# Kernel tuning notes

Measured on AMD Instinct MI355X. Metric: run time of the kernel, lower is better.

Reference implementation:

```python
import jax, jax.numpy as jnp
import numpy as np

# Config: options = {hid_size:1280, num_lstm_layers:2, vocab_size:32000, dropout:0}
L, B, S, H, V = 2, 2, 512, 1280, 32000
C = H  # cell_size == hidden_size == input_size in BiLMEncoder(hid, hid, hid, L)


def setup_inputs() -> dict:
    key = jax.random.key(0)
    ks = jax.random.split(key, 11)
    sc = jnp.float32(0.05)
    def p(k, shape):
        return jax.random.normal(k, shape, dtype=jnp.float32) * sc
    return {
        "x": jax.random.normal(ks[0], (B, S, H), dtype=jnp.float32),
        "Wi_f": p(ks[1], (L, H, 4 * C)),   # input_linearity (no bias)
        "Ws_f": p(ks[2], (L, H, 4 * C)),   # state_linearity
        "b_f":  p(ks[3], (L, 4 * C)),      # state_linearity bias
        "Wp_f": p(ks[4], (L, C, H)),       # state_projection (no bias)
        "Wi_b": p(ks[5], (L, H, 4 * C)),
        "Ws_b": p(ks[6], (L, H, 4 * C)),
        "b_b":  p(ks[7], (L, 4 * C)),
        "Wp_b": p(ks[8], (L, C, H)),
        "W_lin": p(ks[9], (H, V)),
        "b_lin": p(ks[10], (V,)),
    }


def _lstm_dir(x, Wi, Ws, b, Wp, reverse):
    """LstmCellWithProjection over time. x: (B,S,H) -> (B,S,H)."""
    if reverse:
        x = x[:, ::-1, :]
    xp = jnp.einsum('bsh,hk->sbk', x, Wi)  # precompute input projections (S,B,4C)
    h0 = jnp.zeros((x.shape[0], H), x.dtype)
    c0 = jnp.zeros((x.shape[0], C), x.dtype)

    def step(carry, xt):
        h, c = carry
        g = xt + h @ Ws + b                      # (B,4C)
        i, f, z, o = jnp.split(g, 4, axis=-1)
        c_new = jax.nn.sigmoid(i) * jnp.tanh(z) + jax.nn.sigmoid(f) * c
        h_new = (jax.nn.sigmoid(o) * jnp.tanh(c_new)) @ Wp  # projected state
        return (h_new, c_new), h_new

    _, ys = jax.lax.scan(step, (h0, c0), xp)
    ys = jnp.transpose(ys, (1, 0, 2))  # (B,S,H)
    if reverse:
        ys = ys[:, ::-1, :]
    return ys


def _bilm(x, Wi_f, Ws_f, b_f, Wp_f, Wi_b, Ws_b, b_b, Wp_b):
    """ElmoLstm stacked bidirectional LSTM-with-projection, all-ones mask."""
    fwd_in, bwd_in = x, x
    outs = []
    for l in range(L):
        f_cache, b_cache = fwd_in, bwd_in
        f_out = _lstm_dir(fwd_in, Wi_f[l], Ws_f[l], b_f[l], Wp_f[l], reverse=False)
        b_out = _lstm_dir(bwd_in, Wi_b[l], Ws_b[l], b_b[l], Wp_b[l], reverse=True)
        if l != 0:  # residual skip between layers (ElmoLstm)
            f_out = f_out + f_cache
            b_out = b_out + b_cache
        fwd_in, bwd_in = f_out, b_out
        outs.append(jnp.concatenate([f_out, b_out], axis=-1))
    return jnp.stack(outs, axis=0)  # (L,B,S,2H)


def reference(x, Wi_f, Ws_f, b_f, Wp_f, Wi_b, Ws_b, b_b, Wp_b, W_lin, b_lin):
    enc = _bilm(x, Wi_f, Ws_f, b_f, Wp_f, Wi_b, Ws_b, b_b, Wp_b)
    fwd, bwd = enc[..., :H], enc[..., H:]
    logits_fwd = (jnp.einsum('lbsh,hv->lbsv', fwd, W_lin) + b_lin).reshape(B * S, -1)
    logits_bwd = (jnp.einsum('lbsh,hv->lbsv', bwd, W_lin) + b_lin).reshape(B * S, -1)
    return jnp.concatenate([logits_fwd, logits_bwd], axis=0)  # (2*B*S, L*V)
```

## Files before the change

kernel.cpp:

```cpp
#include <hip/hip_runtime.h>
#include <hip/hip_fp16.h>
#include <stdint.h>

#define S_LEN 512
#define HD 1280
#define GD 5120
#define VOC 32000

typedef __attribute__((ext_vector_type(8))) short short8;
typedef __attribute__((ext_vector_type(8))) _Float16 half8;
typedef __attribute__((ext_vector_type(4))) float floatx4;
typedef __attribute__((ext_vector_type(2))) _Float16 halfx2;
typedef __attribute__((ext_vector_type(4))) _Float16 halfx4;

#define GLB1 const __attribute__((address_space(1))) void*
#define LDS3 __attribute__((address_space(3))) void*

static __device__ __forceinline__ unsigned short f2h(float f) {
  return __builtin_bit_cast(unsigned short, (_Float16)f);
}
static __device__ __forceinline__ float h2f(unsigned short h) {
  return (float)__builtin_bit_cast(_Float16, h);
}
static __device__ __forceinline__ float tanhf_fast(float x) {
  float xc = fminf(fmaxf(x, -15.f), 15.f);
  float e = __expf(2.f * xc);
  return (e - 1.f) / (e + 1.f);
}
#if __has_builtin(__builtin_amdgcn_fdot2)
static __device__ __forceinline__ float fdot2(halfx2 a, halfx2 b, float c) {
  return __builtin_amdgcn_fdot2(a, b, c, false);
}
#else
static __device__ __forceinline__ float fdot2(halfx2 a, halfx2 b, float c) {
  return c + (float)a[0]*(float)b[0] + (float)a[1]*(float)b[1];
}
#endif

__global__ __launch_bounds__(256)
void transpose_cvt(const float* __restrict__ in, unsigned short* __restrict__ out,
                   int R, int C)
{
  __shared__ float tile[32][33];
  const int c0 = blockIdx.x * 32;
  const int r0 = blockIdx.y * 32;
  const int tx = threadIdx.x & 31;
  const int ty = threadIdx.x >> 5;
#pragma unroll
  for (int p = 0; p < 4; p++) {
    int rl = ty + p * 8;
    tile[rl][tx] = in[(size_t)(r0 + rl) * C + c0 + tx];
  }
  __syncthreads();
#pragma unroll
  for (int p = 0; p < 4; p++) {
    int cl = ty + p * 8;
    out[(size_t)(c0 + cl) * R + r0 + tx] = f2h(tile[tx][cl]);
  }
}

template<int AFP32, int CMODE>
__global__ __launch_bounds__(256, 2)
void gemm_k(const void* __restrict__ Ap, const unsigned short* __restrict__ BTp,
            void* __restrict__ Cp, const float* __restrict__ bias,
            const unsigned short* __restrict__ resid,
            int M, int N, int K, int rev)
{
  __shared__ __align__(16) short As[128 * 32];
  __shared__ __align__(16) short Bs[128 * 32];
  const int tid  = threadIdx.x;
  const int row0 = blockIdx.y * 128;
  const int col0 = blockIdx.x * 128;
  const int lane = tid & 63;
  const int wid  = tid >> 6;
  const int wrow = (wid >> 1) * 64;
  const int wcol = (wid & 1) * 64;
  const int lr   = lane & 15;
  const int gg   = lane >> 4;

  floatx4 acc[4][4];
#pragma unroll
  for (int m = 0; m < 4; m++)
#pragma unroll
    for (int n = 0; n < 4; n++)
      acc[m][n] = (floatx4)0.0f;

  for (int k0 = 0; k0 < K; k0 += 32) {
    __syncthreads();
#pragma unroll
    for (int p = 0; p < 2; p++) {
      int idx = p * 256 + tid;
      int r = idx >> 2, c = idx & 3;
      if constexpr (AFP32) {
        const float* src = (const float*)Ap + (size_t)(row0 + r) * K + k0 + c * 8;
        floatx4 f0 = *(const floatx4*)src;
        floatx4 f1 = *(const floatx4*)(src + 4);
        short8 va;
        va[0] = (short)f2h(f0[0]); va[1] = (short)f2h(f0[1]);
        va[2] = (short)f2h(f0[2]); va[3] = (short)f2h(f0[3]);
        va[4] = (short)f2h(f1[0]); va[5] = (short)f2h(f1[1]);
        va[6] = (short)f2h(f1[2]); va[7] = (short)f2h(f1[3]);
        *(short8*)&As[r * 32 + ((c ^ (r & 3)) * 8)] = va;
      } else {
        const unsigned short* gsa =
          (const unsigned short*)Ap + (size_t)(row0 + r) * K + k0 + ((c ^ (r & 3)) * 8);
        __builtin_amdgcn_global_load_lds((GLB1)gsa, (LDS3)&As[idx * 8], 16, 0, 0);
      }
      const unsigned short* gsb =
        BTp + (size_t)(col0 + r) * K + k0 + ((c ^ (r & 3)) * 8);
      __builtin_amdgcn_global_load_lds((GLB1)gsb, (LDS3)&Bs[idx * 8], 16, 0, 0);
    }
    __syncthreads();
    short8 af[4], bfv[4];
#pragma unroll
    for (int m = 0; m < 4; m++) {
      int r = wrow + m * 16 + lr;
      af[m] = *(const short8*)&As[r * 32 + ((gg ^ (r & 3)) * 8)];
    }
#pragma unroll
    for (int n = 0; n < 4; n++) {
      int c = wcol + n * 16 + lr;
      bfv[n] = *(const short8*)&Bs[c * 32 + ((gg ^ (c & 3)) * 8)];
    }
#pragma unroll
    for (int m = 0; m < 4; m++)
#pragma unroll
      for (int n = 0; n < 4; n++)
        acc[m][n] = __builtin_amdgcn_mfma_f32_16x16x32_f16(
            __builtin_bit_cast(half8, af[m]), __builtin_bit_cast(half8, bfv[n]),
            acc[m][n], 0, 0, 0);
  }

#pragma unroll
  for (int m = 0; m < 4; m++) {
    int rbase = row0 + wrow + m * 16 + 4 * gg;
#pragma unroll
    for (int n = 0; n < 4; n++) {
      int col = col0 + wcol + n * 16 + lr;
      if constexpr (CMODE == 1) {
        halfx4 t4;
#pragma unroll
        for (int i = 0; i < 4; i++) t4[i] = (_Float16)acc[m][n][i];
        *(halfx4*)((_Float16*)Cp + (size_t)col * M + rbase) = t4;
      } else if constexpr (CMODE == 0) {
        float bv = bias[col];
#pragma unroll
        for (int i = 0; i < 4; i++) {
          int r = rbase + i;
          int b = r >> 9, s = r & 511;
          int so = rev ? (511 - s) : s;
          ((float*)Cp)[(size_t)((so << 1) | b) * GD + col] = acc[m][n][i] + bv;
        }
      } else if constexpr (CMODE == 2) {
#pragma unroll
        for (int i = 0; i < 4; i++) {
          int r = rbase + i;
          int t = r >> 1, b = r & 1;
          int s = rev ? (511 - t) : t;
          size_t o = (size_t)((b << 9) | s) * HD + col;
          float v = acc[m][n][i];
          if (resid) v += h2f(resid[o]);
          ((unsigned short*)Cp)[o] = f2h(v);
        }
      } else {
        float bv = bias[col];
#pragma unroll
        for (int i = 0; i < 4; i++)
          ((float*)Cp)[(size_t)(rbase + i) * N + col] = acc[m][n][i] + bv;
      }
    }
  }
}

__global__ __launch_bounds__(256, 1)
void lstm_scan(const _Float16* __restrict__ wfT,
               const float* __restrict__ xp,
               unsigned short* __restrict__ Pout,
               unsigned int* __restrict__ pbuf,
               unsigned int* __restrict__ ctr,
               int tbase)
{
  const int dir = blockIdx.x & 1;
  const int g   = blockIdx.x >> 1;
  const int jbase = g * 10;
  const int tid = threadIdx.x;
  const int ks  = tid & 31;
  const int cg  = tid >> 5;

  __shared__ __align__(16) unsigned int wlds[40 * 640];
  __shared__ __align__(16) unsigned int plds[1280];
  __shared__ float gvals[40][2];

#pragma unroll 1
  for (int i = 0; i < 25; i++) {
    int idx = i * 256 + tid;
    int c = idx / 160, r = idx - c * 160;
    size_t rowIdx = (size_t)dir * GD + (c / 10) * HD + jbase + (c % 10);
    const uint4* src = (const uint4*)(wfT + rowIdx * HD);
    *(uint4*)&wlds[c * 640 + r * 4] = src[r];
  }

  int gcol[5];
#pragma unroll
  for (int i = 0; i < 5; i++) {
    int c = cg * 5 + i;
    gcol[i] = (c / 10) * HD + jbase + (c % 10);
  }
  const bool isRed = (ks == 0);

  const bool isOwn = tid < 10;
  const int ob = tid & 1;
  const int op = tid >> 1;
  float cst0 = 0.f, cst1 = 0.f;

  __syncthreads();

  for (int t = 0; t < S_LEN; t++) {
    float xpv[5][2];
    if (isRed) {
#pragma unroll
      for (int i = 0; i < 5; i++)
#pragma unroll
        for (int b = 0; b < 2; b++)
          xpv[i][b] = xp[((size_t)dir * 1024 + t * 2 + b) * GD + gcol[i]];
    }

    if (t > 0) {
      if (tid < 64) {
        const unsigned tgt = (unsigned)(tbase + t) * 4u;
        const unsigned int* cp = ctr + dir * 32 + (tid & 31);
        while (true) {
          unsigned v = __hip_atomic_load(cp, __ATOMIC_RELAXED, __HIP_MEMORY_SCOPE_AGENT);
          if (__all(v >= tgt)) break;
          __builtin_amdgcn_s_sleep(1);
        }
      }
      __syncthreads();
    }

    const unsigned int* pr = pbuf + (dir * 2 + (t & 1)) * 1280;
#pragma unroll
    for (int r = 0; r < 5; r++)
      plds[r * 256 + tid] = __hip_atomic_load(pr + r * 256 + tid,
                                              __ATOMIC_RELAXED, __HIP_MEMORY_SCOPE_AGENT);
    __syncthreads();

    float acc[5][2];
#pragma unroll
    for (int i = 0; i < 5; i++) { acc[i][0] = 0.f; acc[i][1] = 0.f; }
#pragma unroll
    for (int j = 0; j < 5; j++) {
      half8 pv0 = *(const half8*)&plds[0 * 640 + ks * 20 + j * 4];
      half8 pv1 = *(const half8*)&plds[1 * 640 + ks * 20 + j * 4];
#pragma unroll
      for (int i = 0; i < 5; i++) {
        half8 wv = *(const half8*)&wlds[(cg * 5 + i) * 640 + ks * 20 + j * 4];
#pragma unroll
        for (int u = 0; u < 4; u++) {
          halfx2 w2  = {wv[2 * u], wv[2 * u + 1]};
          halfx2 p02 = {pv0[2 * u], pv0[2 * u + 1]};
          halfx2 p12 = {pv1[2 * u], pv1[2 * u + 1]};
          acc[i][0] = fdot2(p02, w2, acc[i][0]);
          acc[i][1] = fdot2(p12, w2, acc[i][1]);
        }
      }
    }

#pragma unroll
    for (int i = 0; i < 5; i++)
#pragma unroll
      for (int b = 0; b < 2; b++) {
        float v = acc[i][b];
#pragma unroll
        for (int off = 16; off >= 1; off >>= 1)
          v += __shfl_xor(v, off, 32);
        if (isRed) gvals[cg * 5 + i][b] = v + xpv[i][b];
      }
    __syncthreads();

    unsigned packed = 0;
    if (isOwn) {
      int j0 = op * 2, j1 = op * 2 + 1;
      float gi0 = gvals[j0][ob],      gi1 = gvals[j1][ob];
      float gf0 = gvals[10 + j0][ob], gf1 = gvals[10 + j1][ob];
      float gz0 = gvals[20 + j0][ob], gz1 = gvals[20 + j1][ob];
      float go0 = gvals[30 + j0][ob], go1 = gvals[30 + j1][ob];
      float si0 = 1.f / (1.f + __expf(-gi0)), si1 = 1.f / (1.f + __expf(-gi1));
      float sf0 = 1.f / (1.f + __expf(-gf0)), sf1 = 1.f / (1.f + __expf(-gf1));
      float so0 = 1.f / (1.f + __expf(-go0)), so1 = 1.f / (1.f + __expf(-go1));
      cst0 = si0 * tanhf_fast(gz0) + sf0 * cst0;
      cst1 = si1 * tanhf_fast(gz1) + sf1 * cst1;
      float pv0 = so0 * tanhf_fast(cst0);
      float pv1 = so1 * tanhf_fast(cst1);
      packed = (unsigned)f2h(pv0) | ((unsigned)f2h(pv1) << 16);
      unsigned int* pw = pbuf + (dir * 2 + ((t + 1) & 1)) * 1280;
      __hip_atomic_store(pw + ob * 640 + (jbase >> 1) + op, packed,
                         __ATOMIC_RELAXED, __HIP_MEMORY_SCOPE_AGENT);
    }
    asm volatile("s_waitcnt vmcnt(0)" ::: "memory");
    if (tid == 0) {
      __hip_atomic_fetch_add(ctr + dir * 32 + (g & 31), 1u,
                             __ATOMIC_RELAXED, __HIP_MEMORY_SCOPE_AGENT);
    }
    if (isOwn)
      ((unsigned int*)Pout)[(((size_t)dir * 1024 + t * 2 + ob) * HD + jbase) / 2 + op] = packed;
  }
}

extern "C" void kernel_launch(void* const* d_in, const int* in_sizes, int n_in,
                              void* d_out, int out_size, void* d_ws, size_t ws_size,
                              hipStream_t stream)
{
  char* W = (char*)d_ws;
  const size_t WS_T  = 0;
  const size_t WI_T  = 52428800;
  const size_t WP_T  = 104857600;
  const size_t WF_T  = 117964800;
  const size_t HCAT  = 170393600;
  const size_t P_O   = 180879360;
  const size_t XP_O  = 186122240;
  const size_t PB_O  = 228065280;
  const size_t CTR_O = 228106240;
  const size_t NEED  = 228106496;
  const size_t WLIN_T = 0;
  if (ws_size < NEED) return;

  const float* x    = (const float*)d_in[0];
  const float* Wi_f = (const float*)d_in[1];
  const float* Ws_f = (const float*)d_in[2];
  const float* b_f  = (const float*)d_in[3];
  const float* Wp_f = (const float*)d_in[4];
  const float* Wi_b = (const float*)d_in[5];
  const float* Ws_b = (const float*)d_in[6];
  const float* b_b  = (const float*)d_in[7];
  const float* Wp_b = (const float*)d_in[8];
  const float* Wlin = (const float*)d_in[9];
  const float* blin = (const float*)d_in[10];

  hipMemsetAsync(W + PB_O, 0, 40960 + 256, stream);

  for (int l = 0; l < 2; l++)
    for (int d = 0; d < 2; d++) {
      int ld = l * 2 + d;
      const float* ws_src = (d ? Ws_b : Ws_f) + (size_t)l * HD * GD;
      const float* wi_src = (d ? Wi_b : Wi_f) + (size_t)l * HD * GD;
      const float* wp_src = (d ? Wp_b : Wp_f) + (size_t)l * HD * HD;
      transpose_cvt<<<dim3(GD / 32, HD / 32), 256, 0, stream>>>(
        ws_src, (unsigned short*)(W + WS_T) + (size_t)ld * GD * HD, HD, GD);
      transpose_cvt<<<dim3(GD / 32, HD / 32), 256, 0, stream>>>(
        wi_src, (unsigned short*)(W + WI_T) + (size_t)ld * GD * HD, HD, GD);
      transpose_cvt<<<dim3(HD / 32, HD / 32), 256, 0, stream>>>(
        wp_src, (unsigned short*)(W + WP_T) + (size_t)ld * HD * HD, HD, HD);
    }

  for (int l = 0; l < 2; l++)
    for (int d = 0; d < 2; d++) {
      int ld = l * 2 + d;
      const float* wp_src = (d ? Wp_b : Wp_f) + (size_t)l * HD * HD;
      gemm_k<1, 1><<<dim3(GD / 128, HD / 128), 256, 0, stream>>>(
        wp_src, (const unsigned short*)(W + WS_T) + (size_t)ld * GD * HD,
        (void*)((_Float16*)(W + WF_T) + (size_t)ld * GD * HD),
        nullptr, nullptr, HD, GD, HD, 0);
    }

  for (int l = 0; l < 2; l++) {
    for (int d = 0; d < 2; d++) {
      int ld = l * 2 + d;
      const float* bias = (d ? b_b : b_f) + (size_t)l * GD;
      if (l == 0) {
        gemm_k<1, 0><<<dim3(GD / 128, 1024 / 128), 256, 0, stream>>>(
          x, (const unsigned short*)(W + WI_T) + (size_t)ld * GD * HD,
          (void*)((float*)(W + XP_O) + (size_t)d * 1024 * GD),
          bias, nullptr, 1024, GD, HD, d);
      } else {
        const unsigned short* Ain =
          (const unsigned short*)(W + HCAT) + (size_t)(d * 2048 + (l - 1) * 1024) * HD;
        gemm_k<0, 0><<<dim3(GD / 128, 1024 / 128), 256, 0, stream>>>(
          Ain, (const unsigned short*)(W + WI_T) + (size_t)ld * GD * HD,
          (void*)((float*)(W + XP_O) + (size_t)d * 1024 * GD),
          bias, nullptr, 1024, GD, HD, d);
      }
    }
    if (l == 1) {
      transpose_cvt<<<dim3(VOC / 32, HD / 32), 256, 0, stream>>>(
        Wlin, (unsigned short*)(W + WLIN_T), HD, VOC);
    }
    lstm_scan<<<256, 256, 0, stream>>>(
      (const _Float16*)(W + WF_T) + (size_t)l * 2 * GD * HD,
      (const float*)(W + XP_O),
      (unsigned short*)(W + P_O),
      (unsigned int*)(W + PB_O) + (size_t)l * 5120,
      (unsigned int*)(W + CTR_O),
      l * 512);
    for (int d = 0; d < 2; d++) {
      int ld = l * 2 + d;
      const unsigned short* resid = (l == 0) ? nullptr :
        (const unsigned short*)(W + HCAT) + (size_t)(d * 2048 + (l - 1) * 1024) * HD;
      gemm_k<0, 2><<<dim3(HD / 128, 1024 / 128), 256, 0, stream>>>(
        (const unsigned short*)(W + P_O) + (size_t)d * 1024 * HD,
        (const unsigned short*)(W + WP_T) + (size_t)ld * HD * HD,
        (void*)((unsigned short*)(W + HCAT) + (size_t)(d * 2048 + l * 1024) * HD),
        nullptr, resid, 1024, HD, HD, d);
    }
  }

  gemm_k<0, 3><<<dim3(VOC / 128, 4096 / 128), 256, 0, stream>>>(
    (const unsigned short*)(W + HCAT), (const unsigned short*)(W + WLIN_T),
    d_out, blin, nullptr, 4096, VOC, HD, 0);
}
```

Measured before the change: 7.256 ms.

## Fuse both LSTM layers into one wavefront-pipelined persistent scan kernel

Both LSTM layers now run in a single persistent kernel with 768 threads per block. Layer 1 trails layer 0 by one timestep: layer 1's input projection is folded algebraically into a precomputed Wp0·Wi1 matrix that stays in registers, so layer 1 consumes layer 0's pre-projection state directly. This cuts the serial chain from two 512-step scans to about 513 steps and drops the separate layer-1 input GEMM. The cost is heavy register pressure (wg_reg and wf_reg hold about 100 registers), 768-thread blocks, and rounding effects from the folded fp16 weight product.

```diff
diff --git a/kernel.cpp b/kernel.cpp
--- a/kernel.cpp
+++ b/kernel.cpp
@@ -36,6 +36,9 @@
   return c + (float)a[0]*(float)b[0] + (float)a[1]*(float)b[1];
 }
 #endif
+static __device__ __forceinline__ halfx2 u2h2(unsigned int u) {
+  return __builtin_bit_cast(halfx2, u);
+}
 
 __global__ __launch_bounds__(256)
 void transpose_cvt(const float* __restrict__ in, unsigned short* __restrict__ out,
@@ -172,62 +175,100 @@
   }
 }
 
-__global__ __launch_bounds__(256, 1)
-void lstm_scan(const _Float16* __restrict__ wfT,
-               const float* __restrict__ xp,
-               unsigned short* __restrict__ Pout,
-               unsigned int* __restrict__ pbuf,
-               unsigned int* __restrict__ ctr,
-               int tbase)
+__global__ __launch_bounds__(768, 3)
+void lstm_scan2(const _Float16* __restrict__ wf0T,
+                const _Float16* __restrict__ wf1T,
+                const _Float16* __restrict__ wgT,
+                const float* __restrict__ xp,
+                const float* __restrict__ b1f,
+                const float* __restrict__ b1b,
+                unsigned short* __restrict__ Pout0,
+                unsigned short* __restrict__ Pout1,
+                unsigned int* __restrict__ pbuf,
+                unsigned int* __restrict__ ctr)
 {
   const int dir = blockIdx.x & 1;
   const int g   = blockIdx.x >> 1;
   const int jbase = g * 10;
   const int tid = threadIdx.x;
-  const int ks  = tid & 31;
-  const int cg  = tid >> 5;
 
   __shared__ __align__(16) unsigned int wlds[40 * 640];
-  __shared__ __align__(16) unsigned int plds[1280];
-  __shared__ float gvals[40][2];
-
-#pragma unroll 1
-  for (int i = 0; i < 25; i++) {
-    int idx = i * 256 + tid;
-    int c = idx / 160, r = idx - c * 160;
-    size_t rowIdx = (size_t)dir * GD + (c / 10) * HD + jbase + (c % 10);
-    const uint4* src = (const uint4*)(wfT + rowIdx * HD);
-    *(uint4*)&wlds[c * 640 + r * 4] = src[r];
-  }
-
+  __shared__ __align__(16) unsigned int plds[2 * 1280];
+  __shared__ float gvals0[40][2];
+  __shared__ float gvals1[40][2];
+
+  for (int i = 0; i < 9; i++) {
+    int idx = i * 768 + tid;
+    if (idx < 6400) {
+      int c = idx / 160, r = idx - c * 160;
+      size_t rowIdx = (size_t)dir * GD + (c / 10) * HD + jbase + (c % 10);
+      *(uint4*)&wlds[c * 640 + r * 4] = ((const uint4*)(wf0T + rowIdx * HD))[r];
+    }
+  }
+
+  const int ks = tid & 31;
+  const int cg = (tid & 255) >> 5;
   int gcol[5];
 #pragma unroll
   for (int i = 0; i < 5; i++) {
     int c = cg * 5 + i;
     gcol[i] = (c / 10) * HD + jbase + (c % 10);
   }
-  const bool isRed = (ks == 0);
-
-  const bool isOwn = tid < 10;
-  const int ob = tid & 1;
-  const int op = tid >> 1;
-  float cst0 = 0.f, cst1 = 0.f;
+  const bool isRed = (tid < 256) && (ks == 0);
+
+  const int btid = tid - 256;
+  const int wB = btid >> 6;
+  const int lB = btid & 63;
+  unsigned int wg_reg[5][10], wf_reg[5][10];
+  if (tid >= 256) {
+#pragma unroll
+    for (int c = 0; c < 5; c++) {
+      int cc = wB * 5 + c;
+      size_t rowIdx = (size_t)dir * GD + (cc / 10) * HD + jbase + (cc % 10);
+      const unsigned int* sg = (const unsigned int*)(wgT  + rowIdx * HD) + lB * 10;
+      const unsigned int* sf = (const unsigned int*)(wf1T + rowIdx * HD) + lB * 10;
+#pragma unroll
+      for (int i = 0; i < 10; i += 2) {
+        uint2 a = *(const uint2*)(sg + i); wg_reg[c][i] = a.x; wg_reg[c][i + 1] = a.y;
+        uint2 b = *(const uint2*)(sf + i); wf_reg[c][i] = b.x; wf_reg[c][i + 1] = b.y;
+      }
+    }
+  }
+
+  const bool isOwn0 = tid < 10;
+  const int ob0 = tid & 1, op0 = tid >> 1;
+  float c0a = 0.f, c0b = 0.f;
+  const bool isOwn1 = (tid >= 10) && (tid < 20);
+  const int o1 = tid - 10;
+  const int ob1 = o1 & 1, op1 = o1 >> 1;
+  float c1a = 0.f, c1b = 0.f;
+  float b1v[8];
+  if (isOwn1) {
+    const float* b1 = dir ? b1b : b1f;
+#pragma unroll
+    for (int q = 0; q < 4; q++) {
+      b1v[2 * q]     = b1[q * HD + jbase + op1 * 2];
+      b1v[2 * q + 1] = b1[q * HD + jbase + op1 * 2 + 1];
+    }
+  }
 
   __syncthreads();
 
-  for (int t = 0; t < S_LEN; t++) {
+  for (int r = 0; r <= S_LEN; r++) {
     float xpv[5][2];
-    if (isRed) {
+#pragma unroll
+    for (int i = 0; i < 5; i++) { xpv[i][0] = 0.f; xpv[i][1] = 0.f; }
+    if (isRed && r < S_LEN) {
 #pragma unroll
       for (int i = 0; i < 5; i++)
 #pragma unroll
         for (int b = 0; b < 2; b++)
-          xpv[i][b] = xp[((size_t)dir * 1024 + t * 2 + b) * GD + gcol[i]];
-    }
-
-    if (t > 0) {
+          xpv[i][b] = xp[((size_t)dir * 1024 + r * 2 + b) * GD + gcol[i]];
+    }
+
+    if (r > 0) {
       if (tid < 64) {
-        const unsigned tgt = (unsigned)(tbase + t) * 4u;
+        const unsigned tgt = (unsigned)r * 4u;
         const unsigned int* cp = ctr + dir * 32 + (tid & 31);
         while (true) {
           unsigned v = __hip_atomic_load(cp, __ATOMIC_RELAXED, __HIP_MEMORY_SCOPE_AGENT);
@@ -238,72 +279,128 @@
       __syncthreads();
     }
 
-    const unsigned int* pr = pbuf + (dir * 2 + (t & 1)) * 1280;
-#pragma unroll
-    for (int r = 0; r < 5; r++)
-      plds[r * 256 + tid] = __hip_atomic_load(pr + r * 256 + tid,
-                                              __ATOMIC_RELAXED, __HIP_MEMORY_SCOPE_AGENT);
+    const unsigned int* prs = pbuf + (dir * 2 + (r & 1)) * 2560;
+    if (tid < 512) {
+#pragma unroll
+      for (int i = 0; i < 5; i++)
+        plds[i * 512 + tid] = __hip_atomic_load(prs + i * 512 + tid,
+                                                __ATOMIC_RELAXED, __HIP_MEMORY_SCOPE_AGENT);
+    }
     __syncthreads();
 
-    float acc[5][2];
-#pragma unroll
-    for (int i = 0; i < 5; i++) { acc[i][0] = 0.f; acc[i][1] = 0.f; }
-#pragma unroll
-    for (int j = 0; j < 5; j++) {
-      half8 pv0 = *(const half8*)&plds[0 * 640 + ks * 20 + j * 4];
-      half8 pv1 = *(const half8*)&plds[1 * 640 + ks * 20 + j * 4];
-#pragma unroll
-      for (int i = 0; i < 5; i++) {
-        half8 wv = *(const half8*)&wlds[(cg * 5 + i) * 640 + ks * 20 + j * 4];
-#pragma unroll
-        for (int u = 0; u < 4; u++) {
-          halfx2 w2  = {wv[2 * u], wv[2 * u + 1]};
-          halfx2 p02 = {pv0[2 * u], pv0[2 * u + 1]};
-          halfx2 p12 = {pv1[2 * u], pv1[2 * u + 1]};
-          acc[i][0] = fdot2(p02, w2, acc[i][0]);
-          acc[i][1] = fdot2(p12, w2, acc[i][1]);
+    if (tid < 256) {
+      float acc[5][2];
+#pragma unroll
+      for (int i = 0; i < 5; i++) { acc[i][0] = 0.f; acc[i][1] = 0.f; }
+#pragma unroll
+      for (int j = 0; j < 5; j++) {
+        half8 pv0 = *(const half8*)&plds[0 * 640 + ks * 20 + j * 4];
+        half8 pv1 = *(const half8*)&plds[1 * 640 + ks * 20 + j * 4];
+#pragma unroll
+        for (int i = 0; i < 5; i++) {
+          half8 wv = *(const half8*)&wlds[(cg * 5 + i) * 640 + ks * 20 + j * 4];
+#pragma unroll
+          for (int u = 0; u < 4; u++) {
+            halfx2 w2  = {wv[2 * u], wv[2 * u + 1]};
+            halfx2 p02 = {pv0[2 * u], pv0[2 * u + 1]};
+            halfx2 p12 = {pv1[2 * u], pv1[2 * u + 1]};
+            acc[i][0] = fdot2(p02, w2, acc[i][0]);
+            acc[i][1] = fdot2(p12, w2, acc[i][1]);
+          }
         }
       }
-    }
-
-#pragma unroll
-    for (int i = 0; i < 5; i++)
+#pragma unroll
+      for (int i = 0; i < 5; i++)
+#pragma unroll
+        for (int b = 0; b < 2; b++) {
+          float v = acc[i][b];
+#pragma unroll
+          for (int off = 16; off >= 1; off >>= 1)
+            v += __shfl_xor(v, off, 32);
+          if (isRed) gvals0[cg * 5 + i][b] = v + xpv[i][b];
+        }
+    } else {
+      float acc[5][2];
+#pragma unroll
+      for (int c = 0; c < 5; c++) { acc[c][0] = 0.f; acc[c][1] = 0.f; }
 #pragma unroll
       for (int b = 0; b < 2; b++) {
-        float v = acc[i][b];
-#pragma unroll
-        for (int off = 16; off >= 1; off >>= 1)
-          v += __shfl_xor(v, off, 32);
-        if (isRed) gvals[cg * 5 + i][b] = v + xpv[i][b];
+        unsigned int p0c[10], p1c[10];
+#pragma unroll
+        for (int i = 0; i < 10; i++) {
+          p0c[i] = plds[b * 640 + lB * 10 + i];
+          p1c[i] = plds[1280 + b * 640 + lB * 10 + i];
+        }
+#pragma unroll
+        for (int c = 0; c < 5; c++) {
+          float a = acc[c][b];
+#pragma unroll
+          for (int i = 0; i < 10; i++) {
+            a = fdot2(u2h2(p0c[i]), u2h2(wg_reg[c][i]), a);
+            a = fdot2(u2h2(p1c[i]), u2h2(wf_reg[c][i]), a);
+          }
+          acc[c][b] = a;
+        }
       }
+#pragma unroll
+      for (int c = 0; c < 5; c++)
+#pragma unroll
+        for (int b = 0; b < 2; b++) {
+          float v = acc[c][b];
+#pragma unroll
+          for (int off = 32; off >= 1; off >>= 1)
+            v += __shfl_xor(v, off, 64);
+          if (lB == 0) gvals1[wB * 5 + c][b] = v;
+        }
+    }
     __syncthreads();
 
-    unsigned packed = 0;
-    if (isOwn) {
-      int j0 = op * 2, j1 = op * 2 + 1;
-      float gi0 = gvals[j0][ob],      gi1 = gvals[j1][ob];
-      float gf0 = gvals[10 + j0][ob], gf1 = gvals[10 + j1][ob];
-      float gz0 = gvals[20 + j0][ob], gz1 = gvals[20 + j1][ob];
-      float go0 = gvals[30 + j0][ob], go1 = gvals[30 + j1][ob];
+    unsigned packed0 = 0, packed1 = 0;
+    if (isOwn0 && r < S_LEN) {
+      int j0 = op0 * 2, j1 = j0 + 1;
+      float gi0 = gvals0[j0][ob0],      gi1 = gvals0[j1][ob0];
+      float gf0 = gvals0[10 + j0][ob0], gf1 = gvals0[10 + j1][ob0];
+      float gz0 = gvals0[20 + j0][ob0], gz1 = gvals0[20 + j1][ob0];
+      float go0 = gvals0[30 + j0][ob0], go1 = gvals0[30 + j1][ob0];
       float si0 = 1.f / (1.f + __expf(-gi0)), si1 = 1.f / (1.f + __expf(-gi1));
       float sf0 = 1.f / (1.f + __expf(-gf0)), sf1 = 1.f / (1.f + __expf(-gf1));
       float so0 = 1.f / (1.f + __expf(-go0)), so1 = 1.f / (1.f + __expf(-go1));
-      cst0 = si0 * tanhf_fast(gz0) + sf0 * cst0;
-      cst1 = si1 * tanhf_fast(gz1) + sf1 * cst1;
-      float pv0 = so0 * tanhf_fast(cst0);
-      float pv1 = so1 * tanhf_fast(cst1);
-      packed = (unsigned)f2h(pv0) | ((unsigned)f2h(pv1) << 16);
-      unsigned int* pw = pbuf + (dir * 2 + ((t + 1) & 1)) * 1280;
-      __hip_atomic_store(pw + ob * 640 + (jbase >> 1) + op, packed,
-                         __ATOMIC_RELAXED, __HIP_MEMORY_SCOPE_AGENT);
+      c0a = si0 * tanhf_fast(gz0) + sf0 * c0a;
+      c0b = si1 * tanhf_fast(gz1) + sf1 * c0b;
+      float pv0 = so0 * tanhf_fast(c0a);
+      float pv1 = so1 * tanhf_fast(c0b);
+      packed0 = (unsigned)f2h(pv0) | ((unsigned)f2h(pv1) << 16);
+      unsigned int* pw = pbuf + (dir * 2 + ((r + 1) & 1)) * 2560
+                              + 0 + ob0 * 640 + (jbase >> 1) + op0;
+      __hip_atomic_store(pw, packed0, __ATOMIC_RELAXED, __HIP_MEMORY_SCOPE_AGENT);
+    }
+    if (isOwn1 && r >= 1) {
+      int j0 = op1 * 2, j1 = j0 + 1;
+      float gi0 = gvals1[j0][ob1] + b1v[0],      gi1 = gvals1[j1][ob1] + b1v[1];
+      float gf0 = gvals1[10 + j0][ob1] + b1v[2], gf1 = gvals1[10 + j1][ob1] + b1v[3];
+      float gz0 = gvals1[20 + j0][ob1] + b1v[4], gz1 = gvals1[20 + j1][ob1] + b1v[5];
+      float go0 = gvals1[30 + j0][ob1] + b1v[6], go1 = gvals1[30 + j1][ob1] + b1v[7];
+      float si0 = 1.f / (1.f + __expf(-gi0)), si1 = 1.f / (1.f + __expf(-gi1));
+      float sf0 = 1.f / (1.f + __expf(-gf0)), sf1 = 1.f / (1.f + __expf(-gf1));
+      float so0 = 1.f / (1.f + __expf(-go0)), so1 = 1.f / (1.f + __expf(-go1));
+      c1a = si0 * tanhf_fast(gz0) + sf0 * c1a;
+      c1b = si1 * tanhf_fast(gz1) + sf1 * c1b;
+      float pv0 = so0 * tanhf_fast(c1a);
+      float pv1 = so1 * tanhf_fast(c1b);
+      packed1 = (unsigned)f2h(pv0) | ((unsigned)f2h(pv1) << 16);
+      unsigned int* pw = pbuf + (dir * 2 + ((r + 1) & 1)) * 2560
+                              + 1280 + ob1 * 640 + (jbase >> 1) + op1;
+      __hip_atomic_store(pw, packed1, __ATOMIC_RELAXED, __HIP_MEMORY_SCOPE_AGENT);
     }
     asm volatile("s_waitcnt vmcnt(0)" ::: "memory");
     if (tid == 0) {
       __hip_atomic_fetch_add(ctr + dir * 32 + (g & 31), 1u,
                              __ATOMIC_RELAXED, __HIP_MEMORY_SCOPE_AGENT);
     }
-    if (isOwn)
-      ((unsigned int*)Pout)[(((size_t)dir * 1024 + t * 2 + ob) * HD + jbase) / 2 + op] = packed;
+    if (isOwn0 && r < S_LEN)
+      ((unsigned int*)Pout0)[(((size_t)dir * 1024 + r * 2 + ob0) * HD + jbase) / 2 + op0] = packed0;
+    if (isOwn1 && r >= 1)
+      ((unsigned int*)Pout1)[(((size_t)dir * 1024 + (r - 1) * 2 + ob1) * HD + jbase) / 2 + op1] = packed1;
   }
 }
 
@@ -322,7 +419,9 @@
   const size_t PB_O  = 228065280;
   const size_t CTR_O = 228106240;
   const size_t NEED  = 228106496;
-  const size_t WLIN_T = 0;
+  const size_t WG_T  = 0;
+  const size_t P1_O  = 27262976;
+  const size_t WLIN_T= 33554432;
   if (ws_size < NEED) return;
 
   const float* x    = (const float*)d_in[0];
@@ -362,47 +461,52 @@
         (void*)((_Float16*)(W + WF_T) + (size_t)ld * GD * HD),
         nullptr, nullptr, HD, GD, HD, 0);
     }
-
-  for (int l = 0; l < 2; l++) {
-    for (int d = 0; d < 2; d++) {
-      int ld = l * 2 + d;
-      const float* bias = (d ? b_b : b_f) + (size_t)l * GD;
-      if (l == 0) {
-        gemm_k<1, 0><<<dim3(GD / 128, 1024 / 128), 256, 0, stream>>>(
-          x, (const unsigned short*)(W + WI_T) + (size_t)ld * GD * HD,
-          (void*)((float*)(W + XP_O) + (size_t)d * 1024 * GD),
-          bias, nullptr, 1024, GD, HD, d);
-      } else {
-        const unsigned short* Ain =
-          (const unsigned short*)(W + HCAT) + (size_t)(d * 2048 + (l - 1) * 1024) * HD;
-        gemm_k<0, 0><<<dim3(GD / 128, 1024 / 128), 256, 0, stream>>>(
-          Ain, (const unsigned short*)(W + WI_T) + (size_t)ld * GD * HD,
-          (void*)((float*)(W + XP_O) + (size_t)d * 1024 * GD),
-          bias, nullptr, 1024, GD, HD, d);
-      }
-    }
-    if (l == 1) {
-      transpose_cvt<<<dim3(VOC / 32, HD / 32), 256, 0, stream>>>(
-        Wlin, (unsigned short*)(W + WLIN_T), HD, VOC);
-    }
-    lstm_scan<<<256, 256, 0, stream>>>(
-      (const _Float16*)(W + WF_T) + (size_t)l * 2 * GD * HD,
-      (const float*)(W + XP_O),
-      (unsigned short*)(W + P_O),
-      (unsigned int*)(W + PB_O) + (size_t)l * 5120,
-      (unsigned int*)(W + CTR_O),
-      l * 512);
-    for (int d = 0; d < 2; d++) {
-      int ld = l * 2 + d;
-      const unsigned short* resid = (l == 0) ? nullptr :
-        (const unsigned short*)(W + HCAT) + (size_t)(d * 2048 + (l - 1) * 1024) * HD;
-      gemm_k<0, 2><<<dim3(HD / 128, 1024 / 128), 256, 0, stream>>>(
-        (const unsigned short*)(W + P_O) + (size_t)d * 1024 * HD,
-        (const unsigned short*)(W + WP_T) + (size_t)ld * HD * HD,
-        (void*)((unsigned short*)(W + HCAT) + (size_t)(d * 2048 + l * 1024) * HD),
-        nullptr, resid, 1024, HD, HD, d);
-    }
-  }
+  for (int d = 0; d < 2; d++) {
+    const float* wp0_src = (d ? Wp_b : Wp_f);
+    gemm_k<1, 1><<<dim3(GD / 128, HD / 128), 256, 0, stream>>>(
+      wp0_src, (const unsigned short*)(W + WI_T) + (size_t)(2 + d) * GD * HD,
+      (void*)((_Float16*)(W + WG_T) + (size_t)d * GD * HD),
+      nullptr, nullptr, HD, GD, HD, 0);
+  }
+
+  for (int d = 0; d < 2; d++) {
+    const float* bias = (d ? b_b : b_f);
+    gemm_k<1, 0><<<dim3(GD / 128, 1024 / 128), 256, 0, stream>>>(
+      x, (const unsigned short*)(W + WI_T) + (size_t)d * GD * HD,
+      (void*)((float*)(W + XP_O) + (size_t)d * 1024 * GD),
+      bias, nullptr, 1024, GD, HD, d);
+  }
+
+  lstm_scan2<<<256, 768, 0, stream>>>(
+    (const _Float16*)(W + WF_T),
+    (const _Float16*)(W + WF_T) + (size_t)2 * GD * HD,
+    (const _Float16*)(W + WG_T),
+    (const float*)(W + XP_O),
+    b_f + GD, b_b + GD,
+    (unsigned short*)(W + P_O),
+    (unsigned short*)(W + P1_O),
+    (unsigned int*)(W + PB_O),
+    (unsigned int*)(W + CTR_O));
+
+  for (int d = 0; d < 2; d++) {
+    gemm_k<0, 2><<<dim3(HD / 128, 1024 / 128), 256, 0, stream>>>(
+      (const unsigned short*)(W + P_O) + (size_t)d * 1024 * HD,
+      (const unsigned short*)(W + WP_T) + (size_t)d * HD * HD,
+      (void*)((unsigned short*)(W + HCAT) + (size_t)(d * 2048) * HD),
+      nullptr, nullptr, 1024, HD, HD, d);
+  }
+  for (int d = 0; d < 2; d++) {
+    gemm_k<0, 2><<<dim3(HD / 128, 1024 / 128), 256, 0, stream>>>(
+      (const unsigned short*)(W + P1_O) + (size_t)d * 1024 * HD,
+      (const unsigned short*)(W + WP_T) + (size_t)(2 + d) * HD * HD,
+      (void*)((unsigned short*)(W + HCAT) + (size_t)(d * 2048 + 1024) * HD),
+      nullptr,
+      (const unsigned short*)(W + HCAT) + (size_t)(d * 2048) * HD,
+      1024, HD, HD, d);
+  }
+
+  transpose_cvt<<<dim3(VOC / 32, HD / 32), 256, 0, stream>>>(
+    Wlin, (unsigned short*)(W + WLIN_T), HD, VOC);
 
   gemm_k<0, 3><<<dim3(VOC / 128, 4096 / 128), 256, 0, stream>>>(
     (const unsigned short*)(W + HCAT), (const unsigned short*)(W + WLIN_T),
```

New measurement: 12.22 ms. 68.4% more time.
